# Optimization experiments

Measured on AMD Instinct MI355X. Metric: run time of the kernel, lower is better.

## Reference

```python
import jax, jax.numpy as jnp
import numpy as np

N = 11          # neighborhood size
HEADS = 4
DIM = 128
OUT_DIM = 128
HEAD_DIM = DIM // HEADS
LN_EPS = 1e-5


def unfold_neighborhood(x, n=N):
    # x: [B,H,W,C] -> [B,H,W,N,N,C]; matches torch F.unfold semantics:
    # out[b,h,w,i,j,c] = padded[b, h+i, w+j, c]
    B, H, W, C = x.shape
    P = (n - 1) // 2
    xp = jnp.pad(x, ((0, 0), (P, P), (P, P), (0, 0)))
    patches = jnp.stack(
        [xp[:, i:i + H, j:j + W, :] for i in range(n) for j in range(n)],
        axis=3)  # [B,H,W,N*N,C]
    return patches.reshape(B, H, W, n, n, C)


def setup_inputs() -> dict:
    key = jax.random.key(0)
    ks = jax.random.split(key, 6)
    B, H, W = 2, 64, 64
    q = jax.random.normal(ks[0], (B, H, W, DIM), dtype=jnp.float32)
    kv = jax.random.normal(ks[1], (B, H, W, DIM), dtype=jnp.float32)
    pos_enc = jax.random.normal(ks[2], (N, N, DIM), dtype=jnp.float32)
    # mlp: Linear(N*N*heads -> out_dim)
    fan_in = N * N * HEADS
    bound = 1.0 / np.sqrt(fan_in)
    mlp_w = jax.random.uniform(ks[3], (fan_in, OUT_DIM), jnp.float32, -bound, bound)
    mlp_b = jax.random.uniform(ks[4], (OUT_DIM,), jnp.float32, -bound, bound)
    ln_g = jnp.ones((OUT_DIM,), jnp.float32)
    ln_b = jnp.zeros((OUT_DIM,), jnp.float32)
    return {"q": q, "kv": kv, "pos_enc": pos_enc, "mlp_w": mlp_w,
            "mlp_b": mlp_b, "ln_g": ln_g, "ln_b": ln_b}


def reference(q, kv, pos_enc, mlp_w, mlp_b, ln_g, ln_b):
    B, H, W, C = q.shape
    kv_n = unfold_neighborhood(kv, N) + pos_enc            # [B,H,W,N,N,C]
    # faithful raw row-major reinterpretation of (N,N,C) -> (heads, N^2, head_dim)
    kv_mh = kv_n.reshape(B, H, W, HEADS, N * N, HEAD_DIM)
    q_mh = q.reshape(B, H, W, HEADS, HEAD_DIM)
    # per-pixel per-head dot products (note: original never applies scale)
    scores = jnp.einsum('bxyhnd,bxyhd->bxyhn', kv_mh, q_mh)
    scores = scores.reshape(B, H, W, HEADS * N * N)        # [B,H,W,484]
    mlp_out = jax.nn.gelu(scores @ mlp_w + mlp_b, approximate=False)
    # short_cut is Identity since dim == out_dim
    x = q + mlp_out
    mu = jnp.mean(x, axis=-1, keepdims=True)
    var = jnp.mean(jnp.square(x - mu), axis=-1, keepdims=True)
    return (x - mu) * jax.lax.rsqrt(var + LN_EPS) * ln_g + ln_b
```

## Files before the change

### kernel.cpp

```cpp
#include <hip/hip_runtime.h>
#include <math.h>

#define NB 11
#define PAD 5
#define DIM 128
#define NN 121
#define S_TOT 484
#define IMG 64
#define TILE 8
#define PDIM 74
#define SCP 520
#define NT_A 31
#define NPAD (2 * PDIM * PDIM)
#define LN_EPS 1e-5f

typedef __attribute__((ext_vector_type(8))) short bf16x8;
typedef __attribute__((ext_vector_type(4))) float f32x4;

static __device__ __forceinline__ unsigned short f2bf(float f) {
    unsigned u = __float_as_uint(f);
    u += 0x7FFF + ((u >> 16) & 1);
    return (unsigned short)(u >> 16);
}

__global__ __launch_bounds__(64) void prep_kernel(
    const float* __restrict__ kv, const float* __restrict__ w,
    const float* __restrict__ pos, unsigned short* __restrict__ pkvb,
    unsigned short* __restrict__ wfrag, unsigned short* __restrict__ posA)
{
    const int blk  = blockIdx.x;
    const int lane = threadIdx.x;
    if (blk < NPAD) {
        const int b  = blk / (PDIM * PDIM);
        const int rr = blk - b * PDIM * PDIM;
        const int py = rr / PDIM;
        const int px = rr - py * PDIM;
        const int ky = py - PAD, kx = px - PAD;
        unsigned v = 0;
        if ((unsigned)ky < (unsigned)IMG && (unsigned)kx < (unsigned)IMG) {
            const float2 f = *(const float2*)(kv + (((size_t)b * IMG + ky) * IMG + kx) * DIM + 2 * lane);
            v = (unsigned)f2bf(f.x) | ((unsigned)f2bf(f.y) << 16);
        }
        *(unsigned*)(pkvb + (size_t)blk * DIM + 2 * lane) = v;
    } else if (blk < NPAD + 128) {
        const int idx = blk - NPAD;
        const int t   = idx & 15;
        const int n   = ((idx >> 4) << 4) + (lane & 15);
        const int kb  = t * 32 + ((lane >> 4) << 3);
        unsigned short v[8];
        #pragma unroll
        for (int j = 0; j < 8; ++j) {
            const int k = kb + j;
            v[j] = (k < S_TOT) ? f2bf(w[(size_t)k * DIM + n]) : (unsigned short)0;
        }
        *(uint4*)(wfrag + (((size_t)idx * 64 + lane) << 3)) = *(const uint4*)v;
    } else {
        const int mt   = blk - NPAD - 128;
        const int m    = lane & 15, quad = lane >> 4;
        const int p    = 4 * mt + (m >> 2);
        const int r    = m & 3;
        unsigned short v[8];
        #pragma unroll
        for (int j = 0; j < 8; ++j)
            v[j] = (p <= 120) ? f2bf(pos[(size_t)p * DIM + 32 * r + 8 * quad + j])
                              : (unsigned short)0;
        *(uint4*)(posA + (((size_t)mt * 64 + lane) << 3)) = *(const uint4*)v;
    }
}

__global__ __launch_bounds__(512) void nca_kernel(
    const float* __restrict__ q, const unsigned short* __restrict__ pkvb,
    const unsigned short* __restrict__ posA, const unsigned short* __restrict__ wfrag,
    const float* __restrict__ bias, const float* __restrict__ gam,
    const float* __restrict__ bet, float* __restrict__ out)
{
    const int tile = blockIdx.x;
    const int pix0 = tile * TILE;
    const int x0 = pix0 & 63;
    const int y  = (pix0 >> 6) & 63;
    const int b  = pix0 >> 12;
    const int tid = threadIdx.x;

    __shared__ float qs[TILE][DIM];
    __shared__ __align__(16) unsigned short sc_bf[TILE][SCP];
    __shared__ float mlp[TILE][DIM];

    for (int i = tid; i < TILE * DIM; i += 512)
        qs[i >> 7][i & 127] = q[(size_t)pix0 * DIM + i];
    if (tid < TILE * 16)
        sc_bf[tid >> 4][496 + (tid & 15)] = 0;

    {
        const int pix  = tid >> 6;
        const int lane = tid & 63;
        const int m    = lane & 15, quad = lane >> 4;
        const int coff = 32 * (m & 3) + 8 * quad;

        const float* qb = q + ((size_t)(pix0 + pix)) * DIM + coff;
        const float4 f0 = *(const float4*)qb;
        const float4 f1 = *(const float4*)(qb + 4);
        unsigned short bq_[8] = {f2bf(f0.x), f2bf(f0.y), f2bf(f0.z), f2bf(f0.w),
                                 f2bf(f1.x), f2bf(f1.y), f2bf(f1.z), f2bf(f1.w)};
        const bf16x8 bq = *(const bf16x8*)bq_;

        int p = m >> 2, ii = 0, jj = p;
        const unsigned short* kvb = pkvb
            + ((size_t)((b * PDIM + y) * PDIM) + (x0 + pix)) * DIM + coff;
        const unsigned short* pp = posA + ((size_t)lane << 3);

        bf16x8 ak = *(const bf16x8*)(kvb + jj * DIM);
        bf16x8 ap = *(const bf16x8*)(pp);

        for (int t = 0; t < NT_A; ++t) {
            int pn = p + 4, jn = jj + 4, in = ii;
            if (jn >= NB) { jn -= NB; ++in; }
            const int ic = (pn > 120) ? 10 : in;
            const int jc = (pn > 120) ? 10 : jn;
            const bf16x8 nk = *(const bf16x8*)(kvb + (ic * PDIM + jc) * DIM);
            const int tn = (t + 1 < NT_A) ? (t + 1) : t;
            const bf16x8 np = *(const bf16x8*)(pp + tn * 512);

            f32x4 acc = {0.f, 0.f, 0.f, 0.f};
            acc = __builtin_amdgcn_mfma_f32_16x16x32_bf16(ak, bq, acc, 0, 0, 0);
            acc = __builtin_amdgcn_mfma_f32_16x16x32_bf16(ap, bq, acc, 0, 0, 0);

            const int sbase = 16 * t + quad * 4;
            const int h0 = (271 * sbase) >> 15;
            const int h3 = (271 * (sbase + 3)) >> 15;
            if (h0 == h3) {
                if (m == h0) {
                    unsigned short v[4] = {f2bf(acc[0]), f2bf(acc[1]),
                                           f2bf(acc[2]), f2bf(acc[3])};
                    *(uint2*)&sc_bf[pix][sbase] = *(const uint2*)v;
                }
            } else {
                #pragma unroll
                for (int reg = 0; reg < 4; ++reg) {
                    const int s = sbase + reg;
                    const int h = (271 * s) >> 15;
                    if (m == h) sc_bf[pix][s] = f2bf(acc[reg]);
                }
            }
            ak = nk; ap = np; p = pn; ii = in; jj = jn;
        }
    }
    __syncthreads();

    {
        const int wv   = tid >> 6;
        const int lane = tid & 63;
        const int m    = lane & 15;
        const int quad = lane >> 4;
        const unsigned short* bfr = wfrag + (((size_t)(wv * 16) * 64 + lane) << 3);
        const unsigned short* ap  = &sc_bf[m & 7][quad * 8];
        f32x4 acc = {0.f, 0.f, 0.f, 0.f};
        bf16x8 b0 = *(const bf16x8*)(bfr);
        bf16x8 b1 = *(const bf16x8*)(bfr + 512);
        bf16x8 b2 = *(const bf16x8*)(bfr + 1024);
        bf16x8 b3 = *(const bf16x8*)(bfr + 1536);
        #pragma unroll
        for (int t = 0; t < 16; ++t) {
            const bf16x8 a = *(const bf16x8*)(ap + t * 32);
            bf16x8 bn = b3;
            if (t + 4 < 16) bn = *(const bf16x8*)(bfr + (t + 4) * 512);
            acc = __builtin_amdgcn_mfma_f32_16x16x32_bf16(a, b0, acc, 0, 0, 0);
            b0 = b1; b1 = b2; b2 = b3; b3 = bn;
        }
        if (quad < 2) {
            #pragma unroll
            for (int reg = 0; reg < 4; ++reg)
                mlp[quad * 4 + reg][wv * 16 + m] = acc[reg];
        }
    }
    __syncthreads();

    for (int idx = tid; idx < TILE * DIM; idx += 512) {
        const int pix = idx >> 7, cc = idx & 127;
        const float v = mlp[pix][cc] + bias[cc];
        const float gl = 0.5f * v * (1.f + erff(v * 0.70710678118654752f));
        qs[pix][cc] += gl;
    }
    __syncthreads();

    {
        const int lane = tid & 63, wid = tid >> 6;
        const float v0 = qs[wid][lane], v1 = qs[wid][lane + 64];
        float sum = v0 + v1;
        #pragma unroll
        for (int off = 1; off < 64; off <<= 1) sum += __shfl_xor(sum, off, 64);
        const float mean = sum * (1.f / 128.f);
        const float d0 = v0 - mean, d1 = v1 - mean;
        float sq = d0 * d0 + d1 * d1;
        #pragma unroll
        for (int off = 1; off < 64; off <<= 1) sq += __shfl_xor(sq, off, 64);
        const float rstd = rsqrtf(sq * (1.f / 128.f) + LN_EPS);
        float* op = out + (size_t)(pix0 + wid) * DIM;
        op[lane]      = d0 * rstd * gam[lane]      + bet[lane];
        op[lane + 64] = d1 * rstd * gam[lane + 64] + bet[lane + 64];
    }
}

__global__ __launch_bounds__(512) void nca_kernel_nopad(
    const float* __restrict__ q, const float* __restrict__ kvsrc,
    const float* __restrict__ pos, const float* __restrict__ w,
    const float* __restrict__ bias, const float* __restrict__ gam,
    const float* __restrict__ bet, float* __restrict__ out)
{
    const int tile = blockIdx.x;
    const int pix0 = tile * TILE;
    const int x0 = pix0 & 63;
    const int y  = (pix0 >> 6) & 63;
    const int b  = pix0 >> 12;
    const int tid = threadIdx.x;

    __shared__ float qs[TILE][DIM];
    __shared__ float sc[S_TOT][TILE];
    __shared__ float part[4][TILE][DIM];

    for (int i = tid; i < TILE * DIM; i += 512)
        qs[i >> 7][i & 127] = q[(size_t)pix0 * DIM + i];
    __syncthreads();

    {
        const int pix = tid >> 6;
        const int grp = (tid >> 4) & 3;
        const int l16 = tid & 15;
        const int r   = l16 >> 2;
        const int dq  = 8 * (l16 & 3);
        const int ch  = 8 * l16;
        const int xpix = x0 + pix;
        int p = grp, i = 0, j = grp;
        int h = 0, rem = 4 * grp + r;
        const float* kvb  = kvsrc + (size_t)b * IMG * IMG * DIM + ch;
        const float* posb = pos + ch;
        float4 q0 = *(const float4*)(&qs[pix][dq]);
        float4 q1 = *(const float4*)(&qs[pix][dq + 4]);
        for (int it = 0; it < 31; ++it) {
            if (p <= 120) {
                float4 k0 = make_float4(0.f,0.f,0.f,0.f), k1 = k0;
                const int ky = y + i - PAD, kx = xpix + j - PAD;
                if (((unsigned)ky < (unsigned)IMG) && ((unsigned)kx < (unsigned)IMG)) {
                    const float* kp = kvb + (size_t)(ky * IMG + kx) * DIM;
                    k0 = *(const float4*)(kp);
                    k1 = *(const float4*)(kp + 4);
                }
                const float4 p0 = *(const float4*)(posb + (size_t)p * DIM);
                const float4 p1 = *(const float4*)(posb + (size_t)p * DIM + 4);
                float t = (k0.x + p0.x) * q0.x + (k0.y + p0.y) * q0.y
                        + (k0.z + p0.z) * q0.z + (k0.w + p0.w) * q0.w
                        + (k1.x + p1.x) * q1.x + (k1.y + p1.y) * q1.y
                        + (k1.z + p1.z) * q1.z + (k1.w + p1.w) * q1.w;
                t += __shfl_xor(t, 1, 64);
                t += __shfl_xor(t, 2, 64);
                if ((l16 & 3) == 0) sc[4 * p + r][pix] = t;
            }
            p += 4; j += 4;
            if (j >= NB) { j -= NB; ++i; }
            rem += 16;
            if (rem >= NN) {
                rem -= NN; ++h;
                q0 = *(const float4*)(&qs[pix][h * 32 + dq]);
                q1 = *(const float4*)(&qs[pix][h * 32 + dq + 4]);
            }
        }
    }
    __syncthreads();

    {
        const int l  = tid & 63;
        const int wv = tid >> 6;
        const int g  = wv >> 1;
        const int ph = wv & 1;
        const float* wc  = w + (size_t)(g * NN) * DIM + l;
        const float* scp = &sc[g * NN][ph * 4];
        float a00=0,a01=0,a10=0,a11=0,a20=0,a21=0,a30=0,a31=0;
        #pragma unroll 2
        for (int s = 0; s < NN; ++s) {
            const float4 sv = *(const float4*)(scp + s * 8);
            const float w0 = wc[(size_t)s * DIM];
            const float w1 = wc[(size_t)s * DIM + 64];
            a00 += sv.x * w0; a01 += sv.x * w1;
            a10 += sv.y * w0; a11 += sv.y * w1;
            a20 += sv.z * w0; a21 += sv.z * w1;
            a30 += sv.w * w0; a31 += sv.w * w1;
        }
        const int pb = ph * 4;
        part[g][pb+0][l] = a00; part[g][pb+0][l+64] = a01;
        part[g][pb+1][l] = a10; part[g][pb+1][l+64] = a11;
        part[g][pb+2][l] = a20; part[g][pb+2][l+64] = a21;
        part[g][pb+3][l] = a30; part[g][pb+3][l+64] = a31;
    }
    __syncthreads();

    for (int idx = tid; idx < TILE * DIM; idx += 512) {
        const int pix = idx >> 7, cc = idx & 127;
        float v = part[0][pix][cc] + part[1][pix][cc]
                + part[2][pix][cc] + part[3][pix][cc] + bias[cc];
        const float gl = 0.5f * v * (1.f + erff(v * 0.70710678118654752f));
        qs[pix][cc] += gl;
    }
    __syncthreads();

    {
        const int lane = tid & 63, wid = tid >> 6;
        const float v0 = qs[wid][lane], v1 = qs[wid][lane + 64];
        float sum = v0 + v1;
        #pragma unroll
        for (int off = 1; off < 64; off <<= 1) sum += __shfl_xor(sum, off, 64);
        const float mean = sum * (1.f / 128.f);
        const float d0 = v0 - mean, d1 = v1 - mean;
        float sq = d0 * d0 + d1 * d1;
        #pragma unroll
        for (int off = 1; off < 64; off <<= 1) sq += __shfl_xor(sq, off, 64);
        const float rstd = rsqrtf(sq * (1.f / 128.f) + LN_EPS);
        float* op = out + (size_t)(pix0 + wid) * DIM;
        op[lane]      = d0 * rstd * gam[lane]      + bet[lane];
        op[lane + 64] = d1 * rstd * gam[lane + 64] + bet[lane + 64];
    }
}

extern "C" void kernel_launch(void* const* d_in, const int* in_sizes, int n_in,
                              void* d_out, int out_size, void* d_ws, size_t ws_size,
                              hipStream_t stream) {
    const float* q    = (const float*)d_in[0];
    const float* kv   = (const float*)d_in[1];
    const float* pos  = (const float*)d_in[2];
    const float* w    = (const float*)d_in[3];
    const float* bias = (const float*)d_in[4];
    const float* gam  = (const float*)d_in[5];
    const float* bet  = (const float*)d_in[6];
    float* out = (float*)d_out;

    const int n_blocks = 2 * IMG * IMG / TILE;
    const size_t pkvb_bytes  = (size_t)2 * PDIM * PDIM * DIM * sizeof(unsigned short);
    const size_t wfrag_bytes = (size_t)8 * 16 * 64 * 8 * sizeof(unsigned short);
    const size_t posA_bytes  = (size_t)NT_A * 64 * 8 * sizeof(unsigned short);

    if (ws_size >= pkvb_bytes + wfrag_bytes + posA_bytes) {
        unsigned short* pkvb  = (unsigned short*)d_ws;
        unsigned short* wfrag = (unsigned short*)((char*)d_ws + pkvb_bytes);
        unsigned short* posA  = (unsigned short*)((char*)d_ws + pkvb_bytes + wfrag_bytes);
        prep_kernel<<<NPAD + 128 + NT_A, 64, 0, stream>>>(kv, w, pos, pkvb, wfrag, posA);
        nca_kernel<<<n_blocks, 512, 0, stream>>>(q, pkvb, posA, wfrag, bias, gam, bet, out);
    } else {
        nca_kernel_nopad<<<n_blocks, 512, 0, stream>>>(q, kv, pos, w, bias, gam, bet, out);
    }
}
```

Baseline: 104.9 us.

## Restructure score MFMAs to share neighborhood kv tiles across the pixel tile

The score computation is reorganized so that q fragments act as the MFMA A operand covering 4 pixels at a time. The union of the 8-pixel tile's neighborhoods (11x18 cells) is swept as the B operand, so each kv cell is loaded and multiplied once for the whole tile instead of once per pixel. The pos-encoding term is computed separately into an fp32 shared buffer and added when scores are written. The goal is fewer redundant kv loads and MFMAs. In exchange it adds a second shared array, an extra barrier, and many MFMA outputs that are discarded outside each pixel's window.

```diff
diff --git a/kernel.cpp b/kernel.cpp
--- a/kernel.cpp
+++ b/kernel.cpp
@@ -10,7 +10,11 @@
 #define TILE 8
 #define PDIM 74
 #define SCP 520
-#define NT_A 31
+#define PSCP 488
+#define UCOLS 18
+#define UCELLS 198
+#define NT_KV 50
+#define NT_POS 31
 #define NPAD (2 * PDIM * PDIM)
 #define LN_EPS 1e-5f
 
@@ -26,7 +30,7 @@
 __global__ __launch_bounds__(64) void prep_kernel(
     const float* __restrict__ kv, const float* __restrict__ w,
     const float* __restrict__ pos, unsigned short* __restrict__ pkvb,
-    unsigned short* __restrict__ wfrag, unsigned short* __restrict__ posA)
+    unsigned short* __restrict__ wfrag, unsigned short* __restrict__ posB)
 {
     const int blk  = blockIdx.x;
     const int lane = threadIdx.x;
@@ -55,22 +59,22 @@
         }
         *(uint4*)(wfrag + (((size_t)idx * 64 + lane) << 3)) = *(const uint4*)v;
     } else {
-        const int mt   = blk - NPAD - 128;
+        const int nt   = blk - NPAD - 128;
         const int m    = lane & 15, quad = lane >> 4;
-        const int p    = 4 * mt + (m >> 2);
+        const int p    = 4 * nt + (m >> 2);
         const int r    = m & 3;
         unsigned short v[8];
         #pragma unroll
         for (int j = 0; j < 8; ++j)
             v[j] = (p <= 120) ? f2bf(pos[(size_t)p * DIM + 32 * r + 8 * quad + j])
                               : (unsigned short)0;
-        *(uint4*)(posA + (((size_t)mt * 64 + lane) << 3)) = *(const uint4*)v;
+        *(uint4*)(posB + (((size_t)nt * 64 + lane) << 3)) = *(const uint4*)v;
     }
 }
 
 __global__ __launch_bounds__(512) void nca_kernel(
     const float* __restrict__ q, const unsigned short* __restrict__ pkvb,
-    const unsigned short* __restrict__ posA, const unsigned short* __restrict__ wfrag,
+    const unsigned short* __restrict__ posB, const unsigned short* __restrict__ wfrag,
     const float* __restrict__ bias, const float* __restrict__ gam,
     const float* __restrict__ bet, float* __restrict__ out)
 {
@@ -82,66 +86,81 @@
     const int tid = threadIdx.x;
 
     __shared__ float qs[TILE][DIM];
+    __shared__ float psc[TILE][PSCP];
     __shared__ __align__(16) unsigned short sc_bf[TILE][SCP];
     __shared__ float mlp[TILE][DIM];
 
     for (int i = tid; i < TILE * DIM; i += 512)
         qs[i >> 7][i & 127] = q[(size_t)pix0 * DIM + i];
-    if (tid < TILE * 16)
-        sc_bf[tid >> 4][496 + (tid & 15)] = 0;
-
-    {
-        const int pix  = tid >> 6;
+    for (int i = tid; i < TILE * (SCP - S_TOT); i += 512)
+        sc_bf[i / (SCP - S_TOT)][S_TOT + i % (SCP - S_TOT)] = 0;
+
+    {
+        const int wid  = tid >> 6;
         const int lane = tid & 63;
-        const int m    = lane & 15, quad = lane >> 4;
-        const int coff = 32 * (m & 3) + 8 * quad;
-
-        const float* qb = q + ((size_t)(pix0 + pix)) * DIM + coff;
-        const float4 f0 = *(const float4*)qb;
-        const float4 f1 = *(const float4*)(qb + 4);
-        unsigned short bq_[8] = {f2bf(f0.x), f2bf(f0.y), f2bf(f0.z), f2bf(f0.w),
-                                 f2bf(f1.x), f2bf(f1.y), f2bf(f1.z), f2bf(f1.w)};
-        const bf16x8 bq = *(const bf16x8*)bq_;
-
-        int p = m >> 2, ii = 0, jj = p;
-        const unsigned short* kvb = pkvb
-            + ((size_t)((b * PDIM + y) * PDIM) + (x0 + pix)) * DIM + coff;
-        const unsigned short* pp = posA + ((size_t)lane << 3);
-
-        bf16x8 ak = *(const bf16x8*)(kvb + jj * DIM);
-        bf16x8 ap = *(const bf16x8*)(pp);
-
-        for (int t = 0; t < NT_A; ++t) {
-            int pn = p + 4, jn = jj + 4, in = ii;
-            if (jn >= NB) { jn -= NB; ++in; }
-            const int ic = (pn > 120) ? 10 : in;
-            const int jc = (pn > 120) ? 10 : jn;
-            const bf16x8 nk = *(const bf16x8*)(kvb + (ic * PDIM + jc) * DIM);
-            const int tn = (t + 1 < NT_A) ? (t + 1) : t;
-            const bf16x8 np = *(const bf16x8*)(pp + tn * 512);
-
-            f32x4 acc = {0.f, 0.f, 0.f, 0.f};
-            acc = __builtin_amdgcn_mfma_f32_16x16x32_bf16(ak, bq, acc, 0, 0, 0);
-            acc = __builtin_amdgcn_mfma_f32_16x16x32_bf16(ap, bq, acc, 0, 0, 0);
-
-            const int sbase = 16 * t + quad * 4;
-            const int h0 = (271 * sbase) >> 15;
-            const int h3 = (271 * (sbase + 3)) >> 15;
-            if (h0 == h3) {
-                if (m == h0) {
-                    unsigned short v[4] = {f2bf(acc[0]), f2bf(acc[1]),
-                                           f2bf(acc[2]), f2bf(acc[3])};
-                    *(uint2*)&sc_bf[pix][sbase] = *(const uint2*)v;
+        const int n    = lane & 15, quad = lane >> 4;
+        const int mt   = wid & 1;
+        const int w4   = wid >> 1;
+        const int pxl  = 4 * mt + quad;
+
+        const float* qa = q + ((size_t)(pix0 + 4 * mt + (n >> 2))) * DIM
+                            + 32 * (n & 3) + 8 * quad;
+        const float4 fa0 = *(const float4*)qa;
+        const float4 fa1 = *(const float4*)(qa + 4);
+        unsigned short aq_[8] = {f2bf(fa0.x), f2bf(fa0.y), f2bf(fa0.z), f2bf(fa0.w),
+                                 f2bf(fa1.x), f2bf(fa1.y), f2bf(fa1.z), f2bf(fa1.w)};
+        const bf16x8 Aq = *(const bf16x8*)aq_;
+
+        {
+            const unsigned short* pb = posB + ((size_t)lane << 3);
+            int nt = w4;
+            bf16x8 Bc = *(const bf16x8*)(pb + (size_t)nt * 512);
+            while (nt < NT_POS) {
+                const int ntn = nt + 4;
+                bf16x8 Bn = Bc;
+                if (ntn < NT_POS) Bn = *(const bf16x8*)(pb + (size_t)ntn * 512);
+                f32x4 acc = {0.f, 0.f, 0.f, 0.f};
+                acc = __builtin_amdgcn_mfma_f32_16x16x32_bf16(Aq, Bc, acc, 0, 0, 0);
+                const int s = 16 * nt + n;
+                if (s < S_TOT) {
+                    const int h = (271 * s) >> 15;
+                    const float v = (h == 0) ? acc[0] : (h == 1) ? acc[1]
+                                  : (h == 2) ? acc[2] : acc[3];
+                    psc[pxl][s] = v;
                 }
-            } else {
-                #pragma unroll
-                for (int reg = 0; reg < 4; ++reg) {
-                    const int s = sbase + reg;
+                Bc = Bn; nt = ntn;
+            }
+        }
+        __syncthreads();
+
+        {
+            const int r  = n & 3;
+            const int co = 32 * r + 8 * quad;
+            const unsigned short* kvb = pkvb
+                + ((size_t)((b * PDIM + y) * PDIM) + x0) * DIM + co;
+            int c = 4 * w4 + (n >> 2);
+            int i = 0, u = c;
+            int nt = w4;
+            bf16x8 Bc = *(const bf16x8*)(kvb + (size_t)(i * PDIM + u) * DIM);
+            while (nt < NT_KV) {
+                int cn = c + 16, in_ = i, un = u + 16;
+                if (un >= UCOLS) { un -= UCOLS; ++in_; }
+                if (cn > UCELLS - 1) { in_ = 10; un = UCOLS - 1; }
+                bf16x8 Bn = Bc;
+                if (nt + 4 < NT_KV)
+                    Bn = *(const bf16x8*)(kvb + (size_t)(in_ * PDIM + un) * DIM);
+                f32x4 acc = {0.f, 0.f, 0.f, 0.f};
+                acc = __builtin_amdgcn_mfma_f32_16x16x32_bf16(Aq, Bc, acc, 0, 0, 0);
+                const int jr = u - pxl;
+                if ((unsigned)jr < 11u) {
+                    const int s = 44 * i + 4 * jr + r;
                     const int h = (271 * s) >> 15;
-                    if (m == h) sc_bf[pix][s] = f2bf(acc[reg]);
+                    const float v = ((h == 0) ? acc[0] : (h == 1) ? acc[1]
+                                   : (h == 2) ? acc[2] : acc[3]) + psc[pxl][s];
+                    sc_bf[pxl][s] = f2bf(v);
                 }
+                Bc = Bn; c = cn; i = in_; u = un; nt += 4;
             }
-            ak = nk; ap = np; p = pn; ii = in; jj = jn;
         }
     }
     __syncthreads();
@@ -334,14 +353,14 @@
     const int n_blocks = 2 * IMG * IMG / TILE;
     const size_t pkvb_bytes  = (size_t)2 * PDIM * PDIM * DIM * sizeof(unsigned short);
     const size_t wfrag_bytes = (size_t)8 * 16 * 64 * 8 * sizeof(unsigned short);
-    const size_t posA_bytes  = (size_t)NT_A * 64 * 8 * sizeof(unsigned short);
-
-    if (ws_size >= pkvb_bytes + wfrag_bytes + posA_bytes) {
+    const size_t posB_bytes  = (size_t)NT_POS * 64 * 8 * sizeof(unsigned short);
+
+    if (ws_size >= pkvb_bytes + wfrag_bytes + posB_bytes) {
         unsigned short* pkvb  = (unsigned short*)d_ws;
         unsigned short* wfrag = (unsigned short*)((char*)d_ws + pkvb_bytes);
-        unsigned short* posA  = (unsigned short*)((char*)d_ws + pkvb_bytes + wfrag_bytes);
-        prep_kernel<<<NPAD + 128 + NT_A, 64, 0, stream>>>(kv, w, pos, pkvb, wfrag, posA);
-        nca_kernel<<<n_blocks, 512, 0, stream>>>(q, pkvb, posA, wfrag, bias, gam, bet, out);
+        unsigned short* posB  = (unsigned short*)((char*)d_ws + pkvb_bytes + wfrag_bytes);
+        prep_kernel<<<NPAD + 128 + NT_POS, 64, 0, stream>>>(kv, w, pos, pkvb, wfrag, posB);
+        nca_kernel<<<n_blocks, 512, 0, stream>>>(q, pkvb, posB, wfrag, bias, gam, bet, out);
     } else {
         nca_kernel_nopad<<<n_blocks, 512, 0, stream>>>(q, kv, pos, w, bias, gam, bet, out);
     }
```

After: 93.01 us. 1.13x faster.
